# Performance work log

Hardware: AMD Instinct MI355X
Metric: run time of the kernel (lower is better)

Reference implementation:

```python
import jax, jax.numpy as jnp
import numpy as np

N = 50000   # nodes
E = 800000  # edges (before self-loops)
DIN = 128
H, C = 4, 32
HC = H * C  # 128
DE = 3      # edge feature dim
G = 64      # graphs in batch
HID = 32
DOUT = 1
LN_EPS = 1e-5


def setup_inputs() -> dict:
    key = jax.random.key(0)
    ks = iter(jax.random.split(key, 64))
    def nrm(shape, s=0.1):
        return jax.random.normal(next(ks), shape, dtype=jnp.float32) * s
    inp = {}
    inp["x"] = jax.random.normal(next(ks), (N, DIN), dtype=jnp.float32)
    inp["edge_index"] = jax.random.randint(next(ks), (2, E), 0, N, dtype=jnp.int32)
    inp["batch"] = jnp.sort(jax.random.randint(next(ks), (N,), 0, G, dtype=jnp.int32))
    inp["edge_attr"] = jax.random.normal(next(ks), (E, DE), dtype=jnp.float32)
    # GATv2 layers: layer0 in=DIN(128); layers 1,2 in=HC(128)
    for l, din in enumerate([DIN, HC, HC]):
        inp[f"Wl{l}"] = nrm((HC, din)); inp[f"bl{l}"] = jnp.zeros((HC,), jnp.float32)
        inp[f"Wr{l}"] = nrm((HC, din)); inp[f"br{l}"] = jnp.zeros((HC,), jnp.float32)
        inp[f"We{l}"] = nrm((HC, DE))
        inp[f"att{l}"] = nrm((H, C))
        inp[f"bo{l}"] = jnp.zeros((HC,), jnp.float32)
    for l in range(2):
        inp[f"ln{l}_g"] = jnp.ones((HC,), jnp.float32)
        inp[f"ln{l}_b"] = jnp.zeros((HC,), jnp.float32)
    # post-processing MLP: 128->32->32->32->1
    inp["pw1"] = nrm((HID, HC)); inp["pb1"] = jnp.zeros((HID,), jnp.float32)
    inp["pw2"] = nrm((HID, HID)); inp["pb2"] = jnp.zeros((HID,), jnp.float32)
    inp["pw3"] = nrm((HID, HID)); inp["pb3"] = jnp.zeros((HID,), jnp.float32)
    inp["pw4"] = nrm((DOUT, HID)); inp["pb4"] = jnp.zeros((DOUT,), jnp.float32)
    return inp


def _gat_layer(x, src, dst, eattr, Wl, bl, Wr, br, We, att, bo):
    # GATv2Conv (concat heads). x_l from lin_l -> source, x_r from lin_r -> target.
    xl = (x @ Wl.T + bl).reshape(-1, H, C)
    xr = (x @ Wr.T + br).reshape(-1, H, C)
    e = (eattr @ We.T).reshape(-1, H, C)
    m = jax.nn.leaky_relu(xl[src] + xr[dst] + e, negative_slope=0.2)  # [E',H,C]
    s = jnp.einsum('ehc,hc->eh', m, att)                              # [E',H]
    smax = jax.ops.segment_max(s, dst, num_segments=N)
    ex = jnp.exp(s - smax[dst])
    den = jax.ops.segment_sum(ex, dst, num_segments=N)
    alpha = ex / (den[dst] + 1e-16)
    out = jax.ops.segment_sum(alpha[:, :, None] * xl[src], dst, num_segments=N)
    return out.reshape(-1, HC) + bo


def _ln(x, g, b):
    mu = jnp.mean(x, axis=-1, keepdims=True)
    var = jnp.mean((x - mu) ** 2, axis=-1, keepdims=True)
    return (x - mu) * jax.lax.rsqrt(var + LN_EPS) * g + b


def _forward(x, edge_attr, edge_index, batch, p):
    src0, dst0 = edge_index[0], edge_index[1]
    # PyG add_self_loops with fill_value='mean': per-dst-node mean of edge_attr
    cnt = jax.ops.segment_sum(jnp.ones((E,), jnp.float32), dst0, num_segments=N)
    loop_attr = jax.ops.segment_sum(edge_attr, dst0, num_segments=N) / jnp.maximum(cnt, 1.0)[:, None]
    ar = jnp.arange(N, dtype=src0.dtype)
    src = jnp.concatenate([src0, ar]); dst = jnp.concatenate([dst0, ar])
    ea = jnp.concatenate([edge_attr, loop_attr], axis=0)
    embedding = x
    for l in range(3):
        x = _gat_layer(x, src, dst, ea, p[f"Wl{l}"], p[f"bl{l}"], p[f"Wr{l}"],
                       p[f"br{l}"], p[f"We{l}"], p[f"att{l}"], p[f"bo{l}"])
        embedding = x
        x = jax.nn.relu(x)  # dropout inactive (eval)
        if l != 2:
            x = _ln(x, p[f"ln{l}_g"], p[f"ln{l}_b"])
    pooled = jax.ops.segment_max(x, batch, num_segments=G)
    pooled = jnp.where(jnp.isfinite(pooled), pooled, 0.0)
    h = jax.nn.relu(pooled @ p["pw1"].T + p["pb1"])
    h = jax.nn.relu(h @ p["pw2"].T + p["pb2"])
    h = jax.nn.relu(h @ p["pw3"].T + p["pb3"])
    out = h @ p["pw4"].T + p["pb4"]
    return embedding, out


def reference(x, edge_index, batch, edge_attr,
              Wl0, bl0, Wr0, br0, We0, att0, bo0,
              Wl1, bl1, Wr1, br1, We1, att1, bo1,
              Wl2, bl2, Wr2, br2, We2, att2, bo2,
              ln0_g, ln0_b, ln1_g, ln1_b,
              pw1, pb1, pw2, pb2, pw3, pb3, pw4, pb4):
    p = dict(Wl0=Wl0, bl0=bl0, Wr0=Wr0, br0=br0, We0=We0, att0=att0, bo0=bo0,
             Wl1=Wl1, bl1=bl1, Wr1=Wr1, br1=br1, We1=We1, att1=att1, bo1=bo1,
             Wl2=Wl2, bl2=bl2, Wr2=Wr2, br2=br2, We2=We2, att2=att2, bo2=bo2,
             ln0_g=ln0_g, ln0_b=ln0_b, ln1_g=ln1_g, ln1_b=ln1_b,
             pw1=pw1, pb1=pb1, pw2=pw2, pb2=pb2, pw3=pw3, pb3=pb3, pw4=pw4, pb4=pb4)
    return _forward(x, edge_attr, edge_index, batch, p)
```

## Files before the change

kernel.cpp:

```cpp
#include <hip/hip_runtime.h>
#include <math.h>


#define LN_EPS 1e-5f
#define LOG2E 1.44269504088896340736f

typedef short bf16x8 __attribute__((ext_vector_type(8)));
typedef float f32x4 __attribute__((ext_vector_type(4)));

static __device__ __forceinline__ unsigned short f2bf(float f) {
  unsigned int u = __float_as_uint(f);
  u += 0x7fffu + ((u >> 16) & 1u);
  return (unsigned short)(u >> 16);
}

static __device__ __forceinline__ float dpp_sum8(float v) {
  int x;
  x = __builtin_amdgcn_update_dpp(0, __float_as_int(v), 0x0B1, 0xf, 0xf, true);
  v += __int_as_float(x);
  x = __builtin_amdgcn_update_dpp(0, __float_as_int(v), 0x04E, 0xf, 0xf, true);
  v += __int_as_float(x);
  x = __builtin_amdgcn_update_dpp(0, __float_as_int(v), 0x141, 0xf, 0xf, true);
  v += __int_as_float(x);
  return v;
}


__global__ void k_degree(const int* __restrict__ ei, int* __restrict__ cnt, int E) {
  int e = (blockIdx.x * blockDim.x + threadIdx.x) * 4;
  if (e + 3 < E) {
    int4 d = *(const int4*)&ei[E + e];
    atomicAdd(&cnt[d.x], 1);
    atomicAdd(&cnt[d.y], 1);
    atomicAdd(&cnt[d.z], 1);
    atomicAdd(&cnt[d.w], 1);
  } else {
    int lim = min(e + 4, E);
    for (; e < lim; ++e) atomicAdd(&cnt[ei[E + e]], 1);
  }
}

__global__ void k_scan1(const int* __restrict__ cnt, int* __restrict__ bsum, int N) {
  __shared__ int sh[256];
  int t = threadIdx.x;
  int n = blockIdx.x * 256 + t;
  sh[t] = (n < N) ? (cnt[n] + 1) : 0;
  __syncthreads();
  for (int s = 128; s > 0; s >>= 1) {
    if (t < s) sh[t] += sh[t + s];
    __syncthreads();
  }
  if (t == 0) bsum[blockIdx.x] = sh[0];
}

__global__ void k_scan2(int* __restrict__ bsum, int* __restrict__ offs, int nb, int total, int N) {
  __shared__ int sh[256];
  int t = threadIdx.x;
  int v = (t < nb) ? bsum[t] : 0;
  sh[t] = v;
  __syncthreads();
  for (int d = 1; d < 256; d <<= 1) {
    int add = (t >= d) ? sh[t - d] : 0;
    __syncthreads();
    sh[t] += add;
    __syncthreads();
  }
  if (t < nb) bsum[t] = sh[t] - v;
  if (t == 0) offs[N] = total;
}

__global__ void k_scan3(const int* __restrict__ cnt, const int* __restrict__ bsum,
                        int* __restrict__ offs, int N) {
  __shared__ int sh[256];
  int t = threadIdx.x;
  int n = blockIdx.x * 256 + t;
  int v = (n < N) ? (cnt[n] + 1) : 0;
  sh[t] = v;
  __syncthreads();
  for (int d = 1; d < 256; d <<= 1) {
    int add = (t >= d) ? sh[t - d] : 0;
    __syncthreads();
    sh[t] += add;
    __syncthreads();
  }
  if (n < N) offs[n] = bsum[blockIdx.x] + sh[t] - v;
}

__global__ void k_initcur(const int* __restrict__ offs, int* __restrict__ gcur, int nbuk) {
  int t = threadIdx.x;
  if (t < nbuk) gcur[t] = offs[t * 256];
}

#define CHUNK 4096
__global__ __launch_bounds__(256) void k_binA(const int* __restrict__ ei, const float* __restrict__ ea,
                                              int* __restrict__ gcur, float4* __restrict__ staged,
                                              int E, int nbuk) {
  __shared__ int hist[256];
  __shared__ int basebuf[256];
  int t = threadIdx.x;
  int e0 = blockIdx.x * CHUNK;

  hist[t] = 0;
  __syncthreads();
#pragma unroll
  for (int i = 0; i < CHUNK / 256; ++i) {
    int e = e0 + i * 256 + t;
    if (e < E) atomicAdd(&hist[ei[E + e] >> 8], 1);
  }
  __syncthreads();
  int h = hist[t];
  if (t < nbuk && h > 0) basebuf[t] = atomicAdd(&gcur[t], h);
  hist[t] = 0;
  __syncthreads();
#pragma unroll
  for (int i = 0; i < CHUNK / 256; ++i) {
    int e = e0 + i * 256 + t;
    if (e < E) {
      int s = ei[e];
      int d = ei[E + e];
      int b = d >> 8;
      int r = atomicAdd(&hist[b], 1);
      float4 rec;
      rec.x = ea[e * 3 + 0];
      rec.y = ea[e * 3 + 1];
      rec.z = ea[e * 3 + 2];
      rec.w = __int_as_float(s | (d << 16));
      staged[basebuf[b] + r] = rec;
    }
  }
}

__global__ __launch_bounds__(256) void k_binB(const float4* __restrict__ staged,
                                              const int* __restrict__ offs,
                                              float4* __restrict__ e4, int N) {
  __shared__ int cur[256];
  int t = threadIdx.x;
  int n0 = blockIdx.x * 256;
  int n1 = min(n0 + 256, N);
  if (n0 + t < n1) cur[t] = offs[n0 + t];
  int start = offs[n0];
  int cntReal = (offs[n1] - start) - (n1 - n0);
  __syncthreads();
  for (int p = start + t; p < start + cntReal; p += 256) {
    float4 rec = staged[p];
    unsigned int u = (unsigned int)__float_as_int(rec.w);
    int s = (int)(u & 0xffffu);
    int d = (int)(u >> 16);
    int pos = atomicAdd(&cur[d - n0], 1);
    float4 out;
    out.x = rec.x;
    out.y = rec.y;
    out.z = rec.z;
    out.w = __int_as_float(s * 256);
    e4[pos] = out;
  }
}

__global__ void k_selfloop(const int* __restrict__ offs, float4* __restrict__ e4, int N) {
  int idx = blockIdx.x * blockDim.x + threadIdx.x;
  int n = idx >> 2;
  if (n >= N) return;
  int sub = idx & 3;
  int beg = offs[n], last = offs[n + 1] - 1;
  float s0 = 0.f, s1 = 0.f, s2 = 0.f;
  for (int p = beg + sub; p < last; p += 4) {
    float4 v = e4[p];
    s0 += v.x;
    s1 += v.y;
    s2 += v.z;
  }
  s0 += __shfl_xor(s0, 1);
  s1 += __shfl_xor(s1, 1);
  s2 += __shfl_xor(s2, 1);
  s0 += __shfl_xor(s0, 2);
  s1 += __shfl_xor(s1, 2);
  s2 += __shfl_xor(s2, 2);
  if (sub == 0) {
    float invc = 1.0f / fmaxf((float)(last - beg), 1.0f);
    float4 r;
    r.x = s0 * invc;
    r.y = s1 * invc;
    r.z = s2 * invc;
    r.w = __int_as_float(n * 256);
    e4[last] = r;
  }
}


__global__ void k_convx(const float* __restrict__ x, unsigned short* __restrict__ xb, int n) {
  int i = (blockIdx.x * blockDim.x + threadIdx.x) * 4;
  if (i >= n) return;
  float4 v = *(const float4*)&x[i];
  ushort4 o;
  o.x = f2bf(v.x); o.y = f2bf(v.y); o.z = f2bf(v.z); o.w = f2bf(v.w);
  *(ushort4*)&xb[i] = o;
}

__global__ void k_convW(const float* __restrict__ w0, const float* __restrict__ w1,
                        const float* __restrict__ w2, const float* __restrict__ w3,
                        const float* __restrict__ w4, const float* __restrict__ w5,
                        unsigned short* __restrict__ dst) {
  const float* srcs[6] = {w0, w1, w2, w3, w4, w5};
  const float* s = srcs[blockIdx.y];
  int i = blockIdx.x * 256 + threadIdx.x;
  dst[(size_t)blockIdx.y * 16384 + i] = f2bf(s[i]);
}

__global__ __launch_bounds__(256) void k_gemm_mfma(const unsigned short* __restrict__ xb,
                                                   const unsigned short* __restrict__ Wb,
                                                   const float* __restrict__ bl, const float* __restrict__ br,
                                                   unsigned short* __restrict__ xlb,
                                                   unsigned short* __restrict__ xrb, int N) {
  int wave = threadIdx.x >> 6;
  int lane = threadIdx.x & 63;
  int which = blockIdx.y;
  const unsigned short* W = Wb + (size_t)which * 16384;
  const float* bias = which ? br : bl;
  unsigned short* out = which ? xrb : xlb;

  int row0 = (blockIdx.x * 4 + wave) * 16;
  if (row0 >= N) return;
  int m = lane & 15;
  int q = lane >> 4;

  int arow = row0 + m;
  if (arow >= N) arow = N - 1;
  const unsigned short* xrow = xb + (size_t)arow * 128 + q * 8;

  bf16x8 afrag[4];
#pragma unroll
  for (int kt = 0; kt < 4; ++kt) afrag[kt] = *(const bf16x8*)(xrow + kt * 32);

  f32x4 acc[8];
#pragma unroll
  for (int jt = 0; jt < 8; ++jt) acc[jt] = (f32x4){0.f, 0.f, 0.f, 0.f};

  const unsigned short* wbase = W + (size_t)m * 128 + q * 8;
#pragma unroll
  for (int kt = 0; kt < 4; ++kt) {
    bf16x8 a = afrag[kt];
#pragma unroll
    for (int jt = 0; jt < 8; ++jt) {
      bf16x8 b = *(const bf16x8*)(wbase + (size_t)jt * 16 * 128 + kt * 32);
      acc[jt] = __builtin_amdgcn_mfma_f32_16x16x32_bf16(a, b, acc[jt], 0, 0, 0);
    }
  }

#pragma unroll
  for (int jt = 0; jt < 8; ++jt) {
    float bs = bias[jt * 16 + m];
#pragma unroll
    for (int r = 0; r < 4; ++r) {
      int rr = row0 + q * 4 + r;
      if (rr < N) out[(size_t)rr * 128 + jt * 16 + m] = f2bf(acc[jt][r] + bs);
    }
  }
}

__global__ __launch_bounds__(256) void k_agg(const unsigned short* __restrict__ xlb,
                                             const unsigned short* __restrict__ xrb,
                                             const float4* __restrict__ e4,
                                             const int* __restrict__ offs,
                                             const float* __restrict__ We, const float* __restrict__ att,
                                             const float* __restrict__ bo,
                                             const float* __restrict__ lng, const float* __restrict__ lnb,
                                             unsigned short* __restrict__ xnext_bf,
                                             float* __restrict__ emb, int last, int N) {
  int w = (blockIdx.x * blockDim.x + threadIdx.x) >> 6;
  if (w >= N) return;
  int lane = threadIdx.x & 63;
  int half = lane >> 5;
  int sl = lane & 31;
  int c = sl * 4;
  unsigned int c2 = (unsigned int)(c * 2);
  int beg = offs[w], end = offs[w + 1];
  int cnt = end - beg;

  f32x4 xr4, wea, web, wec, at4;
  {
    uint2 vr = *(const uint2*)&xrb[(size_t)w * 128 + c];
    xr4[0] = __uint_as_float(vr.x << 16);
    xr4[1] = __uint_as_float(vr.x & 0xffff0000u);
    xr4[2] = __uint_as_float(vr.y << 16);
    xr4[3] = __uint_as_float(vr.y & 0xffff0000u);
#pragma unroll
    for (int j = 0; j < 4; ++j) {
      wea[j] = We[(c + j) * 3 + 0];
      web[j] = We[(c + j) * 3 + 1];
      wec[j] = We[(c + j) * 3 + 2];
      at4[j] = att[c + j] * LOG2E;
    }
  }

  const char* xlB = (const char*)xlb;
  const char* e4B = (const char*)e4;
  unsigned int lastoff = (unsigned int)(end - 1) << 4;
  unsigned int eoff = (unsigned int)(beg + half) << 4;
  if (eoff > lastoff) eoff = lastoff;

  float l = 0.f;
  f32x4 acc = {0.f, 0.f, 0.f, 0.f};

  int T = (cnt + 1) >> 1;
  float4 eC = *(const float4*)(e4B + eoff);

#pragma unroll 2
  for (int it = 0; it < T - 1; ++it) {
    unsigned int noff = eoff + 32u;
    if (noff > lastoff) noff = lastoff;
    float4 eN = *(const float4*)(e4B + noff);
    eoff = noff;

    unsigned int go = (unsigned int)__float_as_int(eC.w) + c2;
    uint2 v = *(const uint2*)(xlB + go);
    f32x4 xl4;
    xl4[0] = __uint_as_float(v.x << 16);
    xl4[1] = __uint_as_float(v.x & 0xffff0000u);
    xl4[2] = __uint_as_float(v.y << 16);
    xl4[3] = __uint_as_float(v.y & 0xffff0000u);

    f32x4 t = xr4 + wea * eC.x + web * eC.y + wec * eC.z + xl4;
    t[0] = fmaxf(t[0], 0.2f * t[0]);
    t[1] = fmaxf(t[1], 0.2f * t[1]);
    t[2] = fmaxf(t[2], 0.2f * t[2]);
    t[3] = fmaxf(t[3], 0.2f * t[3]);
    float s = t[0] * at4[0] + t[1] * at4[1] + t[2] * at4[2] + t[3] * at4[3];
    float wgt = __builtin_amdgcn_exp2f(dpp_sum8(s));
    l += wgt;
    acc += xl4 * wgt;
    eC = eN;
  }
  {
    int idx = 2 * (T - 1) + half;
    unsigned int go = (unsigned int)__float_as_int(eC.w) + c2;
    uint2 v = *(const uint2*)(xlB + go);
    f32x4 xl4;
    xl4[0] = __uint_as_float(v.x << 16);
    xl4[1] = __uint_as_float(v.x & 0xffff0000u);
    xl4[2] = __uint_as_float(v.y << 16);
    xl4[3] = __uint_as_float(v.y & 0xffff0000u);
    f32x4 t = xr4 + wea * eC.x + web * eC.y + wec * eC.z + xl4;
    t[0] = fmaxf(t[0], 0.2f * t[0]);
    t[1] = fmaxf(t[1], 0.2f * t[1]);
    t[2] = fmaxf(t[2], 0.2f * t[2]);
    t[3] = fmaxf(t[3], 0.2f * t[3]);
    float s = t[0] * at4[0] + t[1] * at4[1] + t[2] * at4[2] + t[3] * at4[3];
    float wgt = __builtin_amdgcn_exp2f(dpp_sum8(s));
    if (idx >= cnt) wgt = 0.f;
    l += wgt;
    acc += xl4 * wgt;
  }

  l += __shfl_xor(l, 32);
  acc[0] += __shfl_xor(acc[0], 32);
  acc[1] += __shfl_xor(acc[1], 32);
  acc[2] += __shfl_xor(acc[2], 32);
  acc[3] += __shfl_xor(acc[3], 32);

  float inv = 1.0f / l;
  f32x4 o;
  const float4 bo4 = *(const float4*)&bo[c];
  o[0] = acc[0] * inv + bo4.x;
  o[1] = acc[1] * inv + bo4.y;
  o[2] = acc[2] * inv + bo4.z;
  o[3] = acc[3] * inv + bo4.w;

  if (last) {
    if (half == 0) {
      float4 st = {o[0], o[1], o[2], o[3]};
      *(float4*)&emb[(size_t)w * 128 + c] = st;
    }
  } else {
    f32x4 r;
    r[0] = fmaxf(o[0], 0.f);
    r[1] = fmaxf(o[1], 0.f);
    r[2] = fmaxf(o[2], 0.f);
    r[3] = fmaxf(o[3], 0.f);
    float s = r[0] + r[1] + r[2] + r[3];
    s += __shfl_xor(s, 1);
    s += __shfl_xor(s, 2);
    s += __shfl_xor(s, 4);
    s += __shfl_xor(s, 8);
    s += __shfl_xor(s, 16);
    float mu = s * 0.0078125f;
    f32x4 d;
    d[0] = r[0] - mu;
    d[1] = r[1] - mu;
    d[2] = r[2] - mu;
    d[3] = r[3] - mu;
    float v2 = d[0] * d[0] + d[1] * d[1] + d[2] * d[2] + d[3] * d[3];
    v2 += __shfl_xor(v2, 1);
    v2 += __shfl_xor(v2, 2);
    v2 += __shfl_xor(v2, 4);
    v2 += __shfl_xor(v2, 8);
    v2 += __shfl_xor(v2, 16);
    float var = v2 * 0.0078125f;
    float rstd = rsqrtf(var + LN_EPS);
    if (half == 0) {
      const float4 g4 = *(const float4*)&lng[c];
      const float4 b4 = *(const float4*)&lnb[c];
      float o0 = d[0] * rstd * g4.x + b4.x;
      float o1 = d[1] * rstd * g4.y + b4.y;
      float o2 = d[2] * rstd * g4.z + b4.z;
      float o3 = d[3] * rstd * g4.w + b4.w;
      uint2 pack;
      pack.x = (unsigned int)f2bf(o0) | ((unsigned int)f2bf(o1) << 16);
      pack.y = (unsigned int)f2bf(o2) | ((unsigned int)f2bf(o3) << 16);
      *(uint2*)&xnext_bf[(size_t)w * 128 + c] = pack;
    }
  }
}

__global__ void k_pool(const float* __restrict__ emb, const int* __restrict__ batch,
                       float* __restrict__ pooled, int N) {
  int c = threadIdx.x & 127;
  int half = threadIdx.x >> 7;
  int base = blockIdx.x * 64 + half;
  int limit = min(blockIdx.x * 64 + 64, N);
  float cur = 0.f;
  int curg = -1;
  for (int n = base; n < limit; n += 2) {
    int g = batch[n];
    if (g != curg) {
      if (curg >= 0) atomicMax((unsigned int*)&pooled[curg * 128 + c], __float_as_uint(cur));
      curg = g;
      cur = 0.f;
    }
    cur = fmaxf(cur, emb[(size_t)n * 128 + c]);
  }
  if (curg >= 0) atomicMax((unsigned int*)&pooled[curg * 128 + c], __float_as_uint(cur));
}

__global__ void k_mlp(const float* __restrict__ pooled,
                      const float* __restrict__ pw1, const float* __restrict__ pb1,
                      const float* __restrict__ pw2, const float* __restrict__ pb2,
                      const float* __restrict__ pw3, const float* __restrict__ pb3,
                      const float* __restrict__ pw4, const float* __restrict__ pb4,
                      float* __restrict__ out) {
  int g = blockIdx.x;
  int t = threadIdx.x;
  __shared__ float buf1[32], buf2[32];
  if (t < 32) {
    float acc = pb1[t];
    for (int k = 0; k < 128; ++k) acc += pw1[t * 128 + k] * pooled[g * 128 + k];
    buf1[t] = fmaxf(acc, 0.f);
  }
  __syncthreads();
  if (t < 32) {
    float acc = pb2[t];
    for (int k = 0; k < 32; ++k) acc += pw2[t * 32 + k] * buf1[k];
    buf2[t] = fmaxf(acc, 0.f);
  }
  __syncthreads();
  if (t < 32) {
    float acc = pb3[t];
    for (int k = 0; k < 32; ++k) acc += pw3[t * 32 + k] * buf2[k];
    buf1[t] = fmaxf(acc, 0.f);
  }
  __syncthreads();
  if (t == 0) {
    float acc = pb4[0];
    for (int k = 0; k < 32; ++k) acc += pw4[k] * buf1[k];
    out[g] = acc;
  }
}


extern "C" void kernel_launch(void* const* d_in, const int* in_sizes, int n_in,
                              void* d_out, int out_size, void* d_ws, size_t ws_size,
                              hipStream_t stream) {
  const float* x_in = (const float*)d_in[0];
  const int* ei = (const int*)d_in[1];
  const int* batch = (const int*)d_in[2];
  const float* ea = (const float*)d_in[3];

  const int N = in_sizes[0] / 128;
  const int E = in_sizes[1] / 2;
  const int EP = E + N;
  const int G = out_size - N * 128;
  const int NBUK = (N + 255) / 256;

  const float *Wl[3], *bl[3], *Wr[3], *br[3], *We[3], *att[3], *bo[3];
  for (int l = 0; l < 3; ++l) {
    Wl[l] = (const float*)d_in[4 + 7 * l];
    bl[l] = (const float*)d_in[5 + 7 * l];
    Wr[l] = (const float*)d_in[6 + 7 * l];
    br[l] = (const float*)d_in[7 + 7 * l];
    We[l] = (const float*)d_in[8 + 7 * l];
    att[l] = (const float*)d_in[9 + 7 * l];
    bo[l] = (const float*)d_in[10 + 7 * l];
  }
  const float* lng[2] = {(const float*)d_in[25], (const float*)d_in[27]};
  const float* lnb[2] = {(const float*)d_in[26], (const float*)d_in[28]};
  const float* pw1 = (const float*)d_in[29];
  const float* pb1 = (const float*)d_in[30];
  const float* pw2 = (const float*)d_in[31];
  const float* pb2 = (const float*)d_in[32];
  const float* pw3 = (const float*)d_in[33];
  const float* pb3 = (const float*)d_in[34];
  const float* pw4 = (const float*)d_in[35];
  const float* pb4 = (const float*)d_in[36];

  char* base = (char*)d_ws;
  size_t cur = 0;
  auto carve = [&](size_t bytes) -> char* {
    char* p = base + cur;
    cur += (bytes + 255) & ~(size_t)255;
    return p;
  };
  unsigned short* xlb = (unsigned short*)carve((size_t)N * 128 * 2);
  unsigned short* xrb = (unsigned short*)carve((size_t)N * 128 * 2);
  unsigned short* xb = (unsigned short*)carve((size_t)N * 128 * 2);
  unsigned short* Wb = (unsigned short*)carve((size_t)6 * 16384 * 2);
  float4* e4 = (float4*)carve((size_t)EP * 16);
  float4* staged = (float4*)carve((size_t)EP * 16);
  int* offs = (int*)carve((size_t)(N + 1) * 4);
  int* cnt = (int*)carve((size_t)N * 4);
  int* gcur = (int*)carve((size_t)(NBUK + 1) * 4);
  int* bsum = (int*)carve(1024);
  float* pooled = (float*)carve((size_t)G * 128 * 4);

  float* emb_out = (float*)d_out;
  float* mlp_out = (float*)d_out + (size_t)N * 128;

  const int NB = (N + 255) / 256;

  hipMemsetAsync(cnt, 0, (size_t)N * 4, stream);
  hipMemsetAsync(pooled, 0, (size_t)G * 128 * 4, stream);

  k_degree<<<(E / 4 + 255) / 256, 256, 0, stream>>>(ei, cnt, E);
  k_scan1<<<NB, 256, 0, stream>>>(cnt, bsum, N);
  k_scan2<<<1, 256, 0, stream>>>(bsum, offs, NB, EP, N);
  k_scan3<<<NB, 256, 0, stream>>>(cnt, bsum, offs, N);
  k_initcur<<<1, 256, 0, stream>>>(offs, gcur, NBUK);
  k_binA<<<(E + CHUNK - 1) / CHUNK, 256, 0, stream>>>(ei, ea, gcur, staged, E, NBUK);
  k_binB<<<NBUK, 256, 0, stream>>>(staged, offs, e4, N);
  k_selfloop<<<(N * 4 + 255) / 256, 256, 0, stream>>>(offs, e4, N);

  k_convx<<<(N * 128 / 4 + 255) / 256, 256, 0, stream>>>(x_in, xb, N * 128);
  {
    dim3 g(64, 6);
    k_convW<<<g, 256, 0, stream>>>(Wl[0], Wr[0], Wl[1], Wr[1], Wl[2], Wr[2], Wb);
  }

  for (int l = 0; l < 3; ++l) {
    dim3 ggrid((N + 63) / 64, 2);
    k_gemm_mfma<<<ggrid, 256, 0, stream>>>(xb, Wb + (size_t)l * 32768, bl[l], br[l], xlb, xrb, N);
    int last = (l == 2) ? 1 : 0;
    const float* g = last ? bo[l] : lng[l];
    const float* b = last ? bo[l] : lnb[l];
    k_agg<<<(N * 64 + 255) / 256, 256, 0, stream>>>(xlb, xrb, e4, offs,
                                                    We[l], att[l], bo[l], g, b,
                                                    xb, emb_out, last, N);
  }

  k_pool<<<(N + 63) / 64, 256, 0, stream>>>(emb_out, batch, pooled, N);
  k_mlp<<<G, 64, 0, stream>>>(pooled, pw1, pb1, pw2, pb2, pw3, pb3, pw4, pb4, mlp_out);
}
```

Before: 530.2 us.

## Build CSR from fixed-capacity bucket staging and widen aggregation to 8 channels per lane

```diff
diff --git a/kernel.cpp b/kernel.cpp
--- a/kernel.cpp
+++ b/kernel.cpp
@@ -4,6 +4,8 @@
 
 #define LN_EPS 1e-5f
 #define LOG2E 1.44269504088896340736f
+#define CHUNK 4096
+#define BCAP 8192
 
 typedef short bf16x8 __attribute__((ext_vector_type(8)));
 typedef float f32x4 __attribute__((ext_vector_type(4)));
@@ -14,86 +16,18 @@
   return (unsigned short)(u >> 16);
 }
 
-static __device__ __forceinline__ float dpp_sum8(float v) {
+static __device__ __forceinline__ float dpp_sum4(float v) {
   int x;
   x = __builtin_amdgcn_update_dpp(0, __float_as_int(v), 0x0B1, 0xf, 0xf, true);
   v += __int_as_float(x);
   x = __builtin_amdgcn_update_dpp(0, __float_as_int(v), 0x04E, 0xf, 0xf, true);
   v += __int_as_float(x);
-  x = __builtin_amdgcn_update_dpp(0, __float_as_int(v), 0x141, 0xf, 0xf, true);
-  v += __int_as_float(x);
   return v;
 }
 
 
-__global__ void k_degree(const int* __restrict__ ei, int* __restrict__ cnt, int E) {
-  int e = (blockIdx.x * blockDim.x + threadIdx.x) * 4;
-  if (e + 3 < E) {
-    int4 d = *(const int4*)&ei[E + e];
-    atomicAdd(&cnt[d.x], 1);
-    atomicAdd(&cnt[d.y], 1);
-    atomicAdd(&cnt[d.z], 1);
-    atomicAdd(&cnt[d.w], 1);
-  } else {
-    int lim = min(e + 4, E);
-    for (; e < lim; ++e) atomicAdd(&cnt[ei[E + e]], 1);
-  }
-}
-
-__global__ void k_scan1(const int* __restrict__ cnt, int* __restrict__ bsum, int N) {
-  __shared__ int sh[256];
-  int t = threadIdx.x;
-  int n = blockIdx.x * 256 + t;
-  sh[t] = (n < N) ? (cnt[n] + 1) : 0;
-  __syncthreads();
-  for (int s = 128; s > 0; s >>= 1) {
-    if (t < s) sh[t] += sh[t + s];
-    __syncthreads();
-  }
-  if (t == 0) bsum[blockIdx.x] = sh[0];
-}
-
-__global__ void k_scan2(int* __restrict__ bsum, int* __restrict__ offs, int nb, int total, int N) {
-  __shared__ int sh[256];
-  int t = threadIdx.x;
-  int v = (t < nb) ? bsum[t] : 0;
-  sh[t] = v;
-  __syncthreads();
-  for (int d = 1; d < 256; d <<= 1) {
-    int add = (t >= d) ? sh[t - d] : 0;
-    __syncthreads();
-    sh[t] += add;
-    __syncthreads();
-  }
-  if (t < nb) bsum[t] = sh[t] - v;
-  if (t == 0) offs[N] = total;
-}
-
-__global__ void k_scan3(const int* __restrict__ cnt, const int* __restrict__ bsum,
-                        int* __restrict__ offs, int N) {
-  __shared__ int sh[256];
-  int t = threadIdx.x;
-  int n = blockIdx.x * 256 + t;
-  int v = (n < N) ? (cnt[n] + 1) : 0;
-  sh[t] = v;
-  __syncthreads();
-  for (int d = 1; d < 256; d <<= 1) {
-    int add = (t >= d) ? sh[t - d] : 0;
-    __syncthreads();
-    sh[t] += add;
-    __syncthreads();
-  }
-  if (n < N) offs[n] = bsum[blockIdx.x] + sh[t] - v;
-}
-
-__global__ void k_initcur(const int* __restrict__ offs, int* __restrict__ gcur, int nbuk) {
-  int t = threadIdx.x;
-  if (t < nbuk) gcur[t] = offs[t * 256];
-}
-
-#define CHUNK 4096
 __global__ __launch_bounds__(256) void k_binA(const int* __restrict__ ei, const float* __restrict__ ea,
-                                              int* __restrict__ gcur, float4* __restrict__ staged,
+                                              int* __restrict__ gcnt, float4* __restrict__ staged,
                                               int E, int nbuk) {
   __shared__ int hist[256];
   __shared__ int basebuf[256];
@@ -109,7 +43,7 @@
   }
   __syncthreads();
   int h = hist[t];
-  if (t < nbuk && h > 0) basebuf[t] = atomicAdd(&gcur[t], h);
+  if (t < nbuk && h > 0) basebuf[t] = t * BCAP + atomicAdd(&gcnt[t], h);
   hist[t] = 0;
   __syncthreads();
 #pragma unroll
@@ -130,58 +64,83 @@
   }
 }
 
+__global__ void k_bscan(const int* __restrict__ gcnt, int* __restrict__ bukStart,
+                        int* __restrict__ offs, int N, int nbuk, int EP) {
+  __shared__ int sh[256];
+  int t = threadIdx.x;
+  int nodes = (t < nbuk) ? min(256, N - t * 256) : 0;
+  int v = (t < nbuk) ? gcnt[t] + nodes : 0;
+  sh[t] = v;
+  __syncthreads();
+  for (int d = 1; d < 256; d <<= 1) {
+    int add = (t >= d) ? sh[t - d] : 0;
+    __syncthreads();
+    sh[t] += add;
+    __syncthreads();
+  }
+  if (t < nbuk) bukStart[t] = sh[t] - v;
+  if (t == 0) offs[N] = EP;
+}
+
 __global__ __launch_bounds__(256) void k_binB(const float4* __restrict__ staged,
-                                              const int* __restrict__ offs,
-                                              float4* __restrict__ e4, int N) {
-  __shared__ int cur[256];
+                                              const int* __restrict__ gcnt,
+                                              const int* __restrict__ bukStart,
+                                              float4* __restrict__ e4,
+                                              int* __restrict__ offs, int N) {
+  __shared__ int hist[256], cur[256], begS[256], sh[256];
   int t = threadIdx.x;
-  int n0 = blockIdx.x * 256;
-  int n1 = min(n0 + 256, N);
-  if (n0 + t < n1) cur[t] = offs[n0 + t];
-  int start = offs[n0];
-  int cntReal = (offs[n1] - start) - (n1 - n0);
-  __syncthreads();
-  for (int p = start + t; p < start + cntReal; p += 256) {
-    float4 rec = staged[p];
+  int b = blockIdx.x;
+  int n0 = b * 256;
+  int nn = min(256, N - n0);
+  int m = gcnt[b];
+  size_t sbase = (size_t)b * BCAP;
+
+  hist[t] = 0;
+  __syncthreads();
+  for (int p = t; p < m; p += 256) {
+    unsigned int u = (unsigned int)__float_as_int(staged[sbase + p].w);
+    atomicAdd(&hist[(int)(u >> 16) - n0], 1);
+  }
+  __syncthreads();
+  int v = (t < nn) ? hist[t] + 1 : 0;
+  sh[t] = v;
+  __syncthreads();
+  for (int d = 1; d < 256; d <<= 1) {
+    int add = (t >= d) ? sh[t - d] : 0;
+    __syncthreads();
+    sh[t] += add;
+    __syncthreads();
+  }
+  if (t < nn) {
+    int base = bukStart[b] + sh[t] - v;
+    cur[t] = base;
+    begS[t] = base;
+    offs[n0 + t] = base;
+  }
+  __syncthreads();
+  for (int p = t; p < m; p += 256) {
+    float4 rec = staged[sbase + p];
     unsigned int u = (unsigned int)__float_as_int(rec.w);
-    int s = (int)(u & 0xffffu);
-    int d = (int)(u >> 16);
-    int pos = atomicAdd(&cur[d - n0], 1);
-    float4 out;
-    out.x = rec.x;
-    out.y = rec.y;
-    out.z = rec.z;
-    out.w = __int_as_float(s * 256);
-    e4[pos] = out;
-  }
-}
-
-__global__ void k_selfloop(const int* __restrict__ offs, float4* __restrict__ e4, int N) {
-  int idx = blockIdx.x * blockDim.x + threadIdx.x;
-  int n = idx >> 2;
-  if (n >= N) return;
-  int sub = idx & 3;
-  int beg = offs[n], last = offs[n + 1] - 1;
-  float s0 = 0.f, s1 = 0.f, s2 = 0.f;
-  for (int p = beg + sub; p < last; p += 4) {
-    float4 v = e4[p];
-    s0 += v.x;
-    s1 += v.y;
-    s2 += v.z;
-  }
-  s0 += __shfl_xor(s0, 1);
-  s1 += __shfl_xor(s1, 1);
-  s2 += __shfl_xor(s2, 1);
-  s0 += __shfl_xor(s0, 2);
-  s1 += __shfl_xor(s1, 2);
-  s2 += __shfl_xor(s2, 2);
-  if (sub == 0) {
+    int pos = atomicAdd(&cur[(int)(u >> 16) - n0], 1);
+    rec.w = __int_as_float((int)(u & 0xffffu) * 256);
+    e4[pos] = rec;
+  }
+  __syncthreads();
+  if (t < nn) {
+    int beg = begS[t], last = cur[t];
+    float s0 = 0.f, s1 = 0.f, s2 = 0.f;
+    for (int p = beg; p < last; ++p) {
+      float4 r = e4[p];
+      s0 += r.x;
+      s1 += r.y;
+      s2 += r.z;
+    }
     float invc = 1.0f / fmaxf((float)(last - beg), 1.0f);
     float4 r;
     r.x = s0 * invc;
     r.y = s1 * invc;
     r.z = s2 * invc;
-    r.w = __int_as_float(n * 256);
+    r.w = __int_as_float((n0 + t) * 256);
     e4[last] = r;
   }
 }
@@ -269,144 +228,179 @@
   int w = (blockIdx.x * blockDim.x + threadIdx.x) >> 6;
   if (w >= N) return;
   int lane = threadIdx.x & 63;
-  int half = lane >> 5;
-  int sl = lane & 31;
-  int c = sl * 4;
+  int grp = lane >> 4;
+  int sl = lane & 15;
+  int c = sl * 8;
   unsigned int c2 = (unsigned int)(c * 2);
   int beg = offs[w], end = offs[w + 1];
   int cnt = end - beg;
 
-  f32x4 xr4, wea, web, wec, at4;
+  float xr8[8];
   {
-    uint2 vr = *(const uint2*)&xrb[(size_t)w * 128 + c];
-    xr4[0] = __uint_as_float(vr.x << 16);
-    xr4[1] = __uint_as_float(vr.x & 0xffff0000u);
-    xr4[2] = __uint_as_float(vr.y << 16);
-    xr4[3] = __uint_as_float(vr.y & 0xffff0000u);
-#pragma unroll
-    for (int j = 0; j < 4; ++j) {
-      wea[j] = We[(c + j) * 3 + 0];
-      web[j] = We[(c + j) * 3 + 1];
-      wec[j] = We[(c + j) * 3 + 2];
-      at4[j] = att[c + j] * LOG2E;
+    uint4 vr = *(const uint4*)&xrb[(size_t)w * 128 + c];
+    xr8[0] = __uint_as_float(vr.x << 16);
+    xr8[1] = __uint_as_float(vr.x & 0xffff0000u);
+    xr8[2] = __uint_as_float(vr.y << 16);
+    xr8[3] = __uint_as_float(vr.y & 0xffff0000u);
+    xr8[4] = __uint_as_float(vr.z << 16);
+    xr8[5] = __uint_as_float(vr.z & 0xffff0000u);
+    xr8[6] = __uint_as_float(vr.w << 16);
+    xr8[7] = __uint_as_float(vr.w & 0xffff0000u);
+  }
+  float wea[8], web[8], wec[8], at8[8];
+  {
+    const float* Wep = We + c * 3;
+#pragma unroll
+    for (int j = 0; j < 8; ++j) {
+      wea[j] = Wep[j * 3 + 0];
+      web[j] = Wep[j * 3 + 1];
+      wec[j] = Wep[j * 3 + 2];
+      at8[j] = att[c + j] * LOG2E;
     }
   }
 
   const char* xlB = (const char*)xlb;
   const char* e4B = (const char*)e4;
   unsigned int lastoff = (unsigned int)(end - 1) << 4;
-  unsigned int eoff = (unsigned int)(beg + half) << 4;
+  unsigned int eoff = (unsigned int)(beg + grp) << 4;
   if (eoff > lastoff) eoff = lastoff;
 
   float l = 0.f;
-  f32x4 acc = {0.f, 0.f, 0.f, 0.f};
-
-  int T = (cnt + 1) >> 1;
+  float acc[8] = {0.f, 0.f, 0.f, 0.f, 0.f, 0.f, 0.f, 0.f};
+
+  int T = (cnt + 3) >> 2;
   float4 eC = *(const float4*)(e4B + eoff);
 
-#pragma unroll 2
   for (int it = 0; it < T - 1; ++it) {
-    unsigned int noff = eoff + 32u;
+    unsigned int noff = eoff + 64u;
     if (noff > lastoff) noff = lastoff;
     float4 eN = *(const float4*)(e4B + noff);
     eoff = noff;
 
     unsigned int go = (unsigned int)__float_as_int(eC.w) + c2;
-    uint2 v = *(const uint2*)(xlB + go);
-    f32x4 xl4;
-    xl4[0] = __uint_as_float(v.x << 16);
-    xl4[1] = __uint_as_float(v.x & 0xffff0000u);
-    xl4[2] = __uint_as_float(v.y << 16);
-    xl4[3] = __uint_as_float(v.y & 0xffff0000u);
-
-    f32x4 t = xr4 + wea * eC.x + web * eC.y + wec * eC.z + xl4;
-    t[0] = fmaxf(t[0], 0.2f * t[0]);
-    t[1] = fmaxf(t[1], 0.2f * t[1]);
-    t[2] = fmaxf(t[2], 0.2f * t[2]);
-    t[3] = fmaxf(t[3], 0.2f * t[3]);
-    float s = t[0] * at4[0] + t[1] * at4[1] + t[2] * at4[2] + t[3] * at4[3];
-    float wgt = __builtin_amdgcn_exp2f(dpp_sum8(s));
+    uint4 v = *(const uint4*)(xlB + go);
+    float xl8[8];
+    xl8[0] = __uint_as_float(v.x << 16);
+    xl8[1] = __uint_as_float(v.x & 0xffff0000u);
+    xl8[2] = __uint_as_float(v.y << 16);
+    xl8[3] = __uint_as_float(v.y & 0xffff0000u);
+    xl8[4] = __uint_as_float(v.z << 16);
+    xl8[5] = __uint_as_float(v.z & 0xffff0000u);
+    xl8[6] = __uint_as_float(v.w << 16);
+    xl8[7] = __uint_as_float(v.w & 0xffff0000u);
+
+    float s = 0.f;
+#pragma unroll
+    for (int j = 0; j < 8; ++j) {
+      float tmp = fmaf(wea[j], eC.x, fmaf(web[j], eC.y, fmaf(wec[j], eC.z, xr8[j]))) + xl8[j];
+      tmp = fmaxf(tmp, 0.2f * tmp);
+      s = fmaf(tmp, at8[j], s);
+    }
+    float wgt = __builtin_amdgcn_exp2f(dpp_sum4(s));
     l += wgt;
-    acc += xl4 * wgt;
+#pragma unroll
+    for (int j = 0; j < 8; ++j) acc[j] = fmaf(wgt, xl8[j], acc[j]);
     eC = eN;
   }
   {
-    int idx = 2 * (T - 1) + half;
+    int idx = 4 * (T - 1) + grp;
     unsigned int go = (unsigned int)__float_as_int(eC.w) + c2;
-    uint2 v = *(const uint2*)(xlB + go);
-    f32x4 xl4;
-    xl4[0] = __uint_as_float(v.x << 16);
-    xl4[1] = __uint_as_float(v.x & 0xffff0000u);
-    xl4[2] = __uint_as_float(v.y << 16);
-    xl4[3] = __uint_as_float(v.y & 0xffff0000u);
-    f32x4 t = xr4 + wea * eC.x + web * eC.y + wec * eC.z + xl4;
-    t[0] = fmaxf(t[0], 0.2f * t[0]);
-    t[1] = fmaxf(t[1], 0.2f * t[1]);
-    t[2] = fmaxf(t[2], 0.2f * t[2]);
-    t[3] = fmaxf(t[3], 0.2f * t[3]);
-    float s = t[0] * at4[0] + t[1] * at4[1] + t[2] * at4[2] + t[3] * at4[3];
-    float wgt = __builtin_amdgcn_exp2f(dpp_sum8(s));
+    uint4 v = *(const uint4*)(xlB + go);
+    float xl8[8];
+    xl8[0] = __uint_as_float(v.x << 16);
+    xl8[1] = __uint_as_float(v.x & 0xffff0000u);
+    xl8[2] = __uint_as_float(v.y << 16);
+    xl8[3] = __uint_as_float(v.y & 0xffff0000u);
+    xl8[4] = __uint_as_float(v.z << 16);
+    xl8[5] = __uint_as_float(v.z & 0xffff0000u);
+    xl8[6] = __uint_as_float(v.w << 16);
+    xl8[7] = __uint_as_float(v.w & 0xffff0000u);
+    float s = 0.f;
+#pragma unroll
+    for (int j = 0; j < 8; ++j) {
+      float tmp = fmaf(wea[j], eC.x, fmaf(web[j], eC.y, fmaf(wec[j], eC.z, xr8[j]))) + xl8[j];
+      tmp = fmaxf(tmp, 0.2f * tmp);
+      s = fmaf(tmp, at8[j], s);
+    }
+    float wgt = __builtin_amdgcn_exp2f(dpp_sum4(s));
     if (idx >= cnt) wgt = 0.f;
     l += wgt;
-    acc += xl4 * wgt;
-  }
-
+#pragma unroll
+    for (int j = 0; j < 8; ++j) acc[j] = fmaf(wgt, xl8[j], acc[j]);
+  }
+
+  l += __shfl_xor(l, 16);
   l += __shfl_xor(l, 32);
-  acc[0] += __shfl_xor(acc[0], 32);
-  acc[1] += __shfl_xor(acc[1], 32);
-  acc[2] += __shfl_xor(acc[2], 32);
-  acc[3] += __shfl_xor(acc[3], 32);
+#pragma unroll
+  for (int j = 0; j < 8; ++j) {
+    acc[j] += __shfl_xor(acc[j], 16);
+    acc[j] += __shfl_xor(acc[j], 32);
+  }
 
   float inv = 1.0f / l;
-  f32x4 o;
-  const float4 bo4 = *(const float4*)&bo[c];
-  o[0] = acc[0] * inv + bo4.x;
-  o[1] = acc[1] * inv + bo4.y;
-  o[2] = acc[2] * inv + bo4.z;
-  o[3] = acc[3] * inv + bo4.w;
+  float o[8];
+  {
+    const float4 b0 = *(const float4*)&bo[c];
+    const float4 b1 = *(const float4*)&bo[c + 4];
+    o[0] = acc[0] * inv + b0.x;
+    o[1] = acc[1] * inv + b0.y;
+    o[2] = acc[2] * inv + b0.z;
+    o[3] = acc[3] * inv + b0.w;
+    o[4] = acc[4] * inv + b1.x;
+    o[5] = acc[5] * inv + b1.y;
+    o[6] = acc[6] * inv + b1.z;
+    o[7] = acc[7] * inv + b1.w;
+  }
 
   if (last) {
-    if (half == 0) {
-      float4 st = {o[0], o[1], o[2], o[3]};
-      *(float4*)&emb[(size_t)w * 128 + c] = st;
+    if (grp == 0) {
+      float4 s0 = {o[0], o[1], o[2], o[3]};
+      float4 s1 = {o[4], o[5], o[6], o[7]};
+      *(float4*)&emb[(size_t)w * 128 + c] = s0;
+      *(float4*)&emb[(size_t)w * 128 + c + 4] = s1;
     }
   } else {
-    f32x4 r;
-    r[0] = fmaxf(o[0], 0.f);
-    r[1] = fmaxf(o[1], 0.f);
-    r[2] = fmaxf(o[2], 0.f);
-    r[3] = fmaxf(o[3], 0.f);
-    float s = r[0] + r[1] + r[2] + r[3];
+    float r[8];
+#pragma unroll
+    for (int j = 0; j < 8; ++j) r[j] = fmaxf(o[j], 0.f);
+    float s = r[0] + r[1] + r[2] + r[3] + r[4] + r[5] + r[6] + r[7];
     s += __shfl_xor(s, 1);
     s += __shfl_xor(s, 2);
     s += __shfl_xor(s, 4);
     s += __shfl_xor(s, 8);
-    s += __shfl_xor(s, 16);
     float mu = s * 0.0078125f;
-    f32x4 d;
-    d[0] = r[0] - mu;
-    d[1] = r[1] - mu;
-    d[2] = r[2] - mu;
-    d[3] = r[3] - mu;
-    float v2 = d[0] * d[0] + d[1] * d[1] + d[2] * d[2] + d[3] * d[3];
+    float d[8];
+    float v2 = 0.f;
+#pragma unroll
+    for (int j = 0; j < 8; ++j) {
+      d[j] = r[j] - mu;
+      v2 = fmaf(d[j], d[j], v2);
+    }
     v2 += __shfl_xor(v2, 1);
     v2 += __shfl_xor(v2, 2);
     v2 += __shfl_xor(v2, 4);
     v2 += __shfl_xor(v2, 8);
-    v2 += __shfl_xor(v2, 16);
     float var = v2 * 0.0078125f;
     float rstd = rsqrtf(var + LN_EPS);
-    if (half == 0) {
-      const float4 g4 = *(const float4*)&lng[c];
-      const float4 b4 = *(const float4*)&lnb[c];
-      float o0 = d[0] * rstd * g4.x + b4.x;
-      float o1 = d[1] * rstd * g4.y + b4.y;
-      float o2 = d[2] * rstd * g4.z + b4.z;
-      float o3 = d[3] * rstd * g4.w + b4.w;
-      uint2 pack;
-      pack.x = (unsigned int)f2bf(o0) | ((unsigned int)f2bf(o1) << 16);
-      pack.y = (unsigned int)f2bf(o2) | ((unsigned int)f2bf(o3) << 16);
-      *(uint2*)&xnext_bf[(size_t)w * 128 + c] = pack;
+    if (grp == 0) {
+      const float4 g0 = *(const float4*)&lng[c];
+      const float4 g1 = *(const float4*)&lng[c + 4];
+      const float4 b0 = *(const float4*)&lnb[c];
+      const float4 b1 = *(const float4*)&lnb[c + 4];
+      float q0 = d[0] * rstd * g0.x + b0.x;
+      float q1 = d[1] * rstd * g0.y + b0.y;
+      float q2 = d[2] * rstd * g0.z + b0.z;
+      float q3 = d[3] * rstd * g0.w + b0.w;
+      float q4 = d[4] * rstd * g1.x + b1.x;
+      float q5 = d[5] * rstd * g1.y + b1.y;
+      float q6 = d[6] * rstd * g1.z + b1.z;
+      float q7 = d[7] * rstd * g1.w + b1.w;
+      uint4 pack;
+      pack.x = (unsigned int)f2bf(q0) | ((unsigned int)f2bf(q1) << 16);
+      pack.y = (unsigned int)f2bf(q2) | ((unsigned int)f2bf(q3) << 16);
+      pack.z = (unsigned int)f2bf(q4) | ((unsigned int)f2bf(q5) << 16);
+      pack.w = (unsigned int)f2bf(q6) | ((unsigned int)f2bf(q7) << 16);
+      *(uint4*)&xnext_bf[(size_t)w * 128 + c] = pack;
     }
   }
 }
@@ -513,29 +507,21 @@
   unsigned short* xb = (unsigned short*)carve((size_t)N * 128 * 2);
   unsigned short* Wb = (unsigned short*)carve((size_t)6 * 16384 * 2);
   float4* e4 = (float4*)carve((size_t)EP * 16);
-  float4* staged = (float4*)carve((size_t)EP * 16);
+  float4* staged = (float4*)carve((size_t)NBUK * BCAP * 16);
   int* offs = (int*)carve((size_t)(N + 1) * 4);
-  int* cnt = (int*)carve((size_t)N * 4);
-  int* gcur = (int*)carve((size_t)(NBUK + 1) * 4);
-  int* bsum = (int*)carve(1024);
+  int* gcnt = (int*)carve((size_t)NBUK * 4);
+  int* bukStart = (int*)carve((size_t)(NBUK + 1) * 4);
   float* pooled = (float*)carve((size_t)G * 128 * 4);
 
   float* emb_out = (float*)d_out;
   float* mlp_out = (float*)d_out + (size_t)N * 128;
 
-  const int NB = (N + 255) / 256;
-
-  hipMemsetAsync(cnt, 0, (size_t)N * 4, stream);
+  hipMemsetAsync(gcnt, 0, (size_t)NBUK * 4, stream);
   hipMemsetAsync(pooled, 0, (size_t)G * 128 * 4, stream);
 
-  k_degree<<<(E / 4 + 255) / 256, 256, 0, stream>>>(ei, cnt, E);
-  k_scan1<<<NB, 256, 0, stream>>>(cnt, bsum, N);
-  k_scan2<<<1, 256, 0, stream>>>(bsum, offs, NB, EP, N);
-  k_scan3<<<NB, 256, 0, stream>>>(cnt, bsum, offs, N);
-  k_initcur<<<1, 256, 0, stream>>>(offs, gcur, NBUK);
-  k_binA<<<(E + CHUNK - 1) / CHUNK, 256, 0, stream>>>(ei, ea, gcur, staged, E, NBUK);
-  k_binB<<<NBUK, 256, 0, stream>>>(staged, offs, e4, N);
-  k_selfloop<<<(N * 4 + 255) / 256, 256, 0, stream>>>(offs, e4, N);
+  k_binA<<<(E + CHUNK - 1) / CHUNK, 256, 0, stream>>>(ei, ea, gcnt, staged, E, NBUK);
+  k_bscan<<<1, 256, 0, stream>>>(gcnt, bukStart, offs, N, NBUK, EP);
+  k_binB<<<NBUK, 256, 0, stream>>>(staged, gcnt, bukStart, e4, offs, N);
 
   k_convx<<<(N * 128 / 4 + 255) / 256, 256, 0, stream>>>(x_in, xb, N * 128);
   {
```

After: 529.1 us. No clear change (-0.2%).
